# Kernel tuning notes

Hardware: AMD Instinct MI355X
Metric: run time of the kernel (lower is better)

The kernel has to match this reference:

```python
import jax, jax.numpy as jnp
import numpy as np

B, C, U, LEN, K = 32, 16, 16, 128, 4  # batch, channels, units, image side, cheb order
POWERS = K + 1


def _path_chebyshev(n, k):
    """Chebyshev polynomials T_0..T_k of the rescaled normalized Laplacian of an
    undirected path graph with n nodes. Returns [k+1, n, n] float32."""
    A = np.zeros((n, n), dtype=np.float64)
    A[np.arange(n - 1), np.arange(1, n)] = 1.0
    A = A + A.T
    d = A.sum(axis=1)
    dinv = 1.0 / np.sqrt(d)
    L = np.eye(n) - dinv[:, None] * A * dinv[None, :]   # normalized Laplacian
    Lt = L - np.eye(n)                                   # rescaled: 2L/lambda_max - I, lambda_max=2
    T = [np.eye(n), Lt]
    for _ in range(2, k + 1):
        T.append(2.0 * Lt @ T[-1] - T[-2])
    return np.stack(T[: k + 1]).astype(np.float32)


def setup_inputs() -> dict:
    key = jax.random.key(0)
    kx, kc = jax.random.split(key)
    x = jax.random.normal(kx, (B, C, LEN, LEN), dtype=jnp.float32)
    coefs = 0.001 * jax.random.normal(kc, (POWERS, POWERS, C, U), dtype=jnp.float32)
    cheb = jnp.asarray(_path_chebyshev(LEN, K))  # same graph for both axes
    return {"x": x, "coefs": coefs, "cheb1": cheb, "cheb2": cheb}


def reference(x, coefs, cheb1, cheb2):
    # out[b,u,p,q] = sum_{k1,k2,c,h,w} coefs[k1,k2,c,u] * cheb1[k1,h,p] * x[b,c,h,w] * cheb2[k2,w,q]
    t1 = jnp.einsum('bchw,khp->bkcpw', x, cheb1)        # apply cheb1 along H
    s = jnp.einsum('bkcpw,klcu->blupw', t1, coefs)      # contract k1 and channels
    out = jnp.einsum('blupw,lwq->bupq', s, cheb2)       # apply cheb2 along W, contract k2
    return out
```

## Files before the change

### kernel.cpp

```cpp
#include <hip/hip_runtime.h>
#include <hip/hip_bf16.h>

#define LEN 128
#define NB 32
#define NC 16
#define NU 16
#define NK 5
#define KC 80
#define KCP 96

typedef unsigned int uint32;
typedef unsigned short ushort16;
typedef __attribute__((ext_vector_type(8))) short bf16x8;
typedef __attribute__((ext_vector_type(4))) float f32x4;

#define MFMA(a, b, c) __builtin_amdgcn_mfma_f32_16x16x32_bf16(a, b, c, 0, 0, 0)

#define SIG(r) (((r) & 15) ^ (((r) >> 3) & 15))

static __device__ inline ushort16 f2bf(float f) {
    union { float f; uint32 u; } v; v.f = f;
    uint32 u = v.u;
    uint32 r = (u + 0x7fffu + ((u >> 16) & 1u)) >> 16;
    return (ushort16)r;
}
static __device__ inline uint32 pkbf(float a, float b) {
    return (uint32)f2bf(a) | ((uint32)f2bf(b) << 16);
}
static __device__ inline bf16x8 frag16(const void* p) {
    return *(const bf16x8*)p;
}

__global__ __launch_bounds__(256) void kprep(const float* __restrict__ x,
                                             const float* __restrict__ coefs,
                                             const float* __restrict__ cheb1,
                                             const float* __restrict__ cheb2,
                                             ushort16* __restrict__ xF,
                                             ushort16* __restrict__ cheb1F,
                                             ushort16* __restrict__ cheb2F,
                                             ushort16* __restrict__ coefF) {
    __shared__ __align__(16) uint32 Xs[128 * 64];
    const int blk = blockIdx.x, tid = threadIdx.x;
    if (blk < 512) {
        const int bc = blk;
        const float* xp = x + (size_t)bc * (LEN * LEN);
        {
            int w = tid & 127, hg = tid >> 7;
            #pragma unroll
            for (int uu = 0; uu < 8; ++uu) {
                int u = hg * 8 + uu;
                uint4 d;
                uint32* dp = (uint32*)&d;
                #pragma unroll
                for (int t = 0; t < 4; ++t) {
                    int h2 = u * 4 + t;
                    dp[t] = pkbf(xp[(2 * h2) * LEN + w], xp[(2 * h2 + 1) * LEN + w]);
                }
                *(uint4*)(Xs + w * 64 + ((u ^ SIG(w)) << 2)) = d;
            }
        }
        __syncthreads();
        ushort16* dst = xF + (size_t)bc * 16384;
        #pragma unroll
        for (int i = 0; i < 8; ++i) {
            int n = tid + i * 256;
            int lane = n & 63, fk = n >> 6;
            int wrow = (fk >> 2) * 16 + (lane & 15);
            int u = (fk & 3) * 4 + (lane >> 4);
            uint4 v = *(const uint4*)(Xs + wrow * 64 + ((u ^ SIG(wrow)) << 2));
            *(uint4*)(dst + (size_t)n * 8) = v;
        }
    } else {
        int i = (blk - 512) * 256 + tid;
        if (i < 81920) {
            int j = i & 7, lane = (i >> 3) & 63, ks = (i >> 9) & 3, nt = i >> 11;
            int kp = nt * 16 + (lane & 15);
            int k = kp >> 7, p = kp & 127;
            int h = ks * 32 + ((lane >> 4) << 3) + j;
            cheb1F[i] = f2bf(cheb1[(k * LEN + h) * LEN + p]);
        } else if (i < 163840) {
            int i2 = i - 81920;
            int j = i2 & 7, lane = (i2 >> 3) & 63, t = i2 >> 9;
            int ks = t % 20, nt = t / 20;
            int q = nt * 16 + (lane & 15);
            int lw = ks * 32 + ((lane >> 4) << 3) + j;
            int l = lw >> 7, w = lw & 127;
            cheb2F[i2] = f2bf(cheb2[(l * LEN + w) * LEN + q]);
        } else {
            int i3 = i - 163840;
            int j = i3 & 7, lane = (i3 >> 3) & 63, t = i3 >> 9;
            int ks = t % 3, nt = t / 3;
            int lu = nt * 16 + (lane & 15);
            int l = lu >> 4, u = lu & 15;
            int kc = ks * 32 + ((lane >> 4) << 3) + j;
            int k = kc >> 4, c = kc & 15;
            coefF[i3] = (kc < KC) ? f2bf(coefs[((k * NK + l) * NC + c) * NU + u]) : (ushort16)0;
        }
    }
}

__global__ __launch_bounds__(256, 4) void k1_mfma(const ushort16* __restrict__ xF,
                                                  const ushort16* __restrict__ cheb1F,
                                                  const float* __restrict__ x,
                                                  ushort16* __restrict__ t1, int b0) {
    __shared__ __align__(16) uint32 Ls[64 * 64];
    __shared__ __align__(16) uint32 Bs[64 * 64];
    const int c = blockIdx.x, bl = blockIdx.y, z = blockIdx.z;
    const int b = b0 + bl;
    const int tid = threadIdx.x;
    const int lane = tid & 63, wave = tid >> 6;
    const int m16 = lane & 15, g = lane >> 4;
    const int wm = wave >> 1, wn = wave & 1;

    #pragma unroll
    for (int i = 0; i < 4; ++i) {
        int u = tid + i * 256;
        int ln = u & 63, ks = (u >> 6) & 3, nt = u >> 8;
        uint4 v = *(const uint4*)(cheb1F + ((size_t)(((8 + z * 4 + nt) * 4 + ks) * 64 + ln)) * 8);
        int row = nt * 16 + (ln & 15), hu = ks * 4 + (ln >> 4);
        *(uint4*)(Ls + row * 64 + ((hu ^ SIG(row)) << 2)) = v;
    }

    if (z == 0) {
        const float* xp = x + (size_t)(b * NC + c) * (LEN * LEN);
        int p = tid >> 1, half = tid & 1;
        const float4* src = (const float4*)(xp + p * LEN + half * 64);
        ushort16* dst = t1 + ((size_t)(bl * LEN + p) * KC + c) * LEN + half * 64;
        #pragma unroll
        for (int i = 0; i < 16; ++i) {
            float4 v = src[i];
            uint2 d;
            d.x = pkbf(v.x, v.y);
            d.y = pkbf(v.z, v.w);
            *(uint2*)(dst + i * 4) = d;
        }
    }
    __syncthreads();

    const ushort16* xFb = xF + ((size_t)(b * NC + c)) * 16384;

    f32x4 acc[4][2];
    #pragma unroll
    for (int mi = 0; mi < 4; ++mi)
        #pragma unroll
        for (int ni = 0; ni < 2; ++ni) acc[mi][ni] = (f32x4)0.f;

    #pragma unroll
    for (int ks = 0; ks < 4; ++ks) {
        bf16x8 Af[4], Bf[2];
        #pragma unroll
        for (int mi = 0; mi < 4; ++mi) {
            int mt = wm * 4 + mi;
            Af[mi] = frag16(xFb + ((size_t)(mt * 4 + ks) * 64 + lane) * 8);
        }
        #pragma unroll
        for (int ni = 0; ni < 2; ++ni) {
            int row = (wn * 2 + ni) * 16 + m16;
            int hu = ks * 4 + g;
            Bf[ni] = frag16(Ls + row * 64 + ((hu ^ SIG(row)) << 2));
        }
        #pragma unroll
        for (int mi = 0; mi < 4; ++mi)
            #pragma unroll
            for (int ni = 0; ni < 2; ++ni)
                acc[mi][ni] = MFMA(Af[mi], Bf[ni], acc[mi][ni]);
    }

    #pragma unroll
    for (int ni = 0; ni < 2; ++ni)
        #pragma unroll
        for (int mi = 0; mi < 4; ++mi) {
            int rr = (wn * 2 + ni) * 16 + m16;
            int wu = (wm * 4 + mi) * 16 + g * 4;
            uint2 d;
            d.x = pkbf(acc[mi][ni][0], acc[mi][ni][1]);
            d.y = pkbf(acc[mi][ni][2], acc[mi][ni][3]);
            int u = wu >> 3;
            *(uint2*)(Bs + rr * 64 + ((u ^ SIG(rr)) << 2) + ((wu >> 1) & 3)) = d;
        }
    __syncthreads();

    #pragma unroll
    for (int i = 0; i < 4; ++i) {
        int n = tid + i * 256;
        int rr = n >> 4, wsg = n & 15;
        uint4 v = *(const uint4*)(Bs + rr * 64 + ((wsg ^ SIG(rr)) << 2));
        int kp = 128 + z * 64 + rr;
        int k = kp >> 7, p = kp & 127;
        *(uint4*)(t1 + ((size_t)((bl * LEN + p) * KC + k * NC + c)) * LEN + wsg * 8) = v;
    }
}

__global__ __launch_bounds__(256, 5) void k2_mfma(const ushort16* __restrict__ t1,
                                                  const ushort16* __restrict__ coefF,
                                                  const ushort16* __restrict__ cheb2F,
                                                  float* __restrict__ out, int b0) {
    __shared__ __align__(16) uint32 sm[128 * 64];
    const int p = blockIdx.x, bl = blockIdx.y, b = b0 + bl;
    const int tid = threadIdx.x;
    const int lane = tid & 63, wave = tid >> 6;
    const int n16 = lane & 15, g = lane >> 4;

    const uint32* t1u = (const uint32*)(t1 + (size_t)(bl * LEN + p) * (KC * LEN));
    uint4 Av[3], Bv[3];
    #pragma unroll
    for (int i = 0; i < 3; ++i) {
        int it = tid + i * 256;
        if (it < 640) {
            int a2 = it >> 4, wq = it & 15;
            const uint32* src = t1u + a2 * 128 + wq * 4;
            Av[i] = *(const uint4*)(src);
            Bv[i] = *(const uint4*)(src + 64);
        }
    }
    #pragma unroll
    for (int i = 0; i < 4; ++i) {
        int idx = tid + i * 256;
        int row = idx >> 3, d = idx & 7;
        int u = 10 + (d >> 2);
        sm[row * 64 + ((u ^ SIG(row)) << 2) + (d & 3)] = 0;
    }
    #pragma unroll
    for (int i = 0; i < 3; ++i) {
        int it = tid + i * 256;
        if (it < 640) {
            int a2 = it >> 4, wq = it & 15;
            const uint32* av = (const uint32*)&Av[i];
            const uint32* bv = (const uint32*)&Bv[i];
            int u = a2 >> 2, lo = a2 & 3;
            #pragma unroll
            for (int j = 0; j < 4; ++j) {
                int r0 = wq * 8 + 2 * j, r1 = r0 + 1;
                sm[r0 * 64 + ((u ^ SIG(r0)) << 2) + lo] = (av[j] & 0xffffu) | (bv[j] << 16);
                sm[r1 * 64 + ((u ^ SIG(r1)) << 2) + lo] = (av[j] >> 16) | (bv[j] & 0xffff0000u);
            }
        }
    }
    __syncthreads();

    f32x4 acc[2][5];
    #pragma unroll
    for (int mi = 0; mi < 2; ++mi)
        #pragma unroll
        for (int ni = 0; ni < 5; ++ni) acc[mi][ni] = (f32x4)0.f;

    #pragma unroll
    for (int ks = 0; ks < 3; ++ks) {
        bf16x8 Af[2], Bf[5];
        #pragma unroll
        for (int mi = 0; mi < 2; ++mi) {
            int row = wave * 32 + mi * 16 + n16;
            Af[mi] = frag16(sm + row * 64 + (((ks * 4 + g) ^ SIG(row)) << 2));
        }
        #pragma unroll
        for (int ni = 0; ni < 5; ++ni)
            Bf[ni] = frag16(coefF + ((size_t)(ni * 3 + ks) * 64 + lane) * 8);
        #pragma unroll
        for (int mi = 0; mi < 2; ++mi)
            #pragma unroll
            for (int ni = 0; ni < 5; ++ni)
                acc[mi][ni] = MFMA(Af[mi], Bf[ni], acc[mi][ni]);
    }
    __syncthreads();

    {
        ushort16* A3 = (ushort16*)sm;
        #pragma unroll
        for (int mi = 0; mi < 2; ++mi)
            #pragma unroll
            for (int ni = 0; ni < 5; ++ni) {
                int wcol = wave * 32 + mi * 16 + g * 4;
                uint2 d;
                d.x = pkbf(acc[mi][ni][0], acc[mi][ni][1]);
                d.y = pkbf(acc[mi][ni][2], acc[mi][ni][3]);
                *(uint2*)(A3 + n16 * 648 + ni * 128 + wcol) = d;
            }
    }
    __syncthreads();

    const ushort16* A3r = (const ushort16*)sm;
    f32x4 c3[2];
    c3[0] = (f32x4)0.f; c3[1] = (f32x4)0.f;
    #pragma unroll 4
    for (int ks = 4; ks < 20; ++ks) {
        bf16x8 Aa = frag16(A3r + n16 * 648 + ks * 32 + g * 8);
        #pragma unroll
        for (int nt = 0; nt < 2; ++nt) {
            bf16x8 Bb = frag16(cheb2F + ((size_t)((wave * 2 + nt) * 20 + ks) * 64 + lane) * 8);
            c3[nt] = MFMA(Aa, Bb, c3[nt]);
        }
    }

    #pragma unroll
    for (int nt = 0; nt < 2; ++nt)
        #pragma unroll
        for (int r = 0; r < 4; ++r) {
            int u = g * 4 + r;
            int q = wave * 32 + nt * 16 + n16;
            uint32 bf = ((uint32)A3r[u * 648 + q]) << 16;
            float l0 = __uint_as_float(bf);
            out[(((size_t)(b * NU + u)) * LEN + p) * LEN + q] = c3[nt][r] + l0;
        }
}

extern "C" void kernel_launch(void* const* d_in, const int* in_sizes, int n_in,
                              void* d_out, int out_size, void* d_ws, size_t ws_size,
                              hipStream_t stream) {
    const float* x     = (const float*)d_in[0];
    const float* coefs = (const float*)d_in[1];
    const float* cheb1 = (const float*)d_in[2];
    const float* cheb2 = (const float*)d_in[3];
    float* out = (float*)d_out;

    const size_t xF_bytes  = (size_t)NB * NC * 16384 * sizeof(ushort16);
    const size_t aux_bytes = 163840 + 163840 + 15360;
    size_t off = (ws_size - aux_bytes - xF_bytes) & ~(size_t)255;
    ushort16* cheb1F = (ushort16*)((char*)d_ws + off);
    ushort16* cheb2F = cheb1F + 81920;
    ushort16* coefF  = cheb2F + 81920;
    ushort16* xF     = coefF + 7680;
    ushort16* t1 = (ushort16*)d_ws;

    const size_t per_b = (size_t)LEN * KC * LEN * sizeof(ushort16);
    int chunk = (int)(off / per_b);
    if (chunk < 1) chunk = 1;
    if (chunk > NB) chunk = NB;

    hipLaunchKernelGGL(kprep, dim3(1182), dim3(256), 0, stream,
                       x, coefs, cheb1, cheb2, xF, cheb1F, cheb2F, coefF);
    for (int b0 = 0; b0 < NB; b0 += chunk) {
        int cb = (NB - b0 < chunk) ? (NB - b0) : chunk;
        hipLaunchKernelGGL(k1_mfma, dim3(NC, cb, 8), dim3(256), 0, stream,
                           xF, cheb1F, x, t1, b0);
        hipLaunchKernelGGL(k2_mfma, dim3(LEN, cb), dim3(256), 0, stream,
                           t1, coefF, cheb2F, out, b0);
    }
}
```

Baseline: 152.6 us.

## Process two p rows per k2 block with cheb2 fragments held in registers

Each k2 block now handles two consecutive p rows instead of one, halving the grid. The cheb2 B fragments are loaded into 32 registers once per block and reused across both rows. The t1 loads for the second row are issued during the first row's compute to overlap memory latency. Launch bounds drop to 2 blocks per SM to fit the much larger register footprint, which reduces occupancy and latency hiding.

```diff
diff --git a/kernel.cpp b/kernel.cpp
--- a/kernel.cpp
+++ b/kernel.cpp
@@ -191,116 +191,142 @@
     }
 }
 
-__global__ __launch_bounds__(256, 5) void k2_mfma(const ushort16* __restrict__ t1,
+__global__ __launch_bounds__(256, 2) void k2_mfma(const ushort16* __restrict__ t1,
                                                   const ushort16* __restrict__ coefF,
                                                   const ushort16* __restrict__ cheb2F,
                                                   float* __restrict__ out, int b0) {
     __shared__ __align__(16) uint32 sm[128 * 64];
-    const int p = blockIdx.x, bl = blockIdx.y, b = b0 + bl;
+    const int pblk = blockIdx.x, bl = blockIdx.y, b = b0 + bl;
     const int tid = threadIdx.x;
     const int lane = tid & 63, wave = tid >> 6;
     const int n16 = lane & 15, g = lane >> 4;
 
-    const uint32* t1u = (const uint32*)(t1 + (size_t)(bl * LEN + p) * (KC * LEN));
+    bf16x8 B3[32];
+    #pragma unroll
+    for (int nt = 0; nt < 2; ++nt)
+        #pragma unroll
+        for (int ks = 4; ks < 20; ++ks)
+            B3[nt * 16 + ks - 4] =
+                frag16(cheb2F + ((size_t)((wave * 2 + nt) * 20 + ks) * 64 + lane) * 8);
+
+    const uint32* t1base = (const uint32*)(t1 + (size_t)(bl * LEN + 2 * pblk) * (KC * LEN));
+
     uint4 Av[3], Bv[3];
     #pragma unroll
     for (int i = 0; i < 3; ++i) {
         int it = tid + i * 256;
         if (it < 640) {
             int a2 = it >> 4, wq = it & 15;
-            const uint32* src = t1u + a2 * 128 + wq * 4;
+            const uint32* src = t1base + a2 * 128 + wq * 4;
             Av[i] = *(const uint4*)(src);
             Bv[i] = *(const uint4*)(src + 64);
         }
     }
-    #pragma unroll
-    for (int i = 0; i < 4; ++i) {
-        int idx = tid + i * 256;
-        int row = idx >> 3, d = idx & 7;
-        int u = 10 + (d >> 2);
-        sm[row * 64 + ((u ^ SIG(row)) << 2) + (d & 3)] = 0;
-    }
-    #pragma unroll
-    for (int i = 0; i < 3; ++i) {
-        int it = tid + i * 256;
-        if (it < 640) {
-            int a2 = it >> 4, wq = it & 15;
-            const uint32* av = (const uint32*)&Av[i];
-            const uint32* bv = (const uint32*)&Bv[i];
-            int u = a2 >> 2, lo = a2 & 3;
-            #pragma unroll
-            for (int j = 0; j < 4; ++j) {
-                int r0 = wq * 8 + 2 * j, r1 = r0 + 1;
-                sm[r0 * 64 + ((u ^ SIG(r0)) << 2) + lo] = (av[j] & 0xffffu) | (bv[j] << 16);
-                sm[r1 * 64 + ((u ^ SIG(r1)) << 2) + lo] = (av[j] >> 16) | (bv[j] & 0xffff0000u);
-            }
-        }
-    }
-    __syncthreads();
-
-    f32x4 acc[2][5];
-    #pragma unroll
-    for (int mi = 0; mi < 2; ++mi)
-        #pragma unroll
-        for (int ni = 0; ni < 5; ++ni) acc[mi][ni] = (f32x4)0.f;
-
-    #pragma unroll
-    for (int ks = 0; ks < 3; ++ks) {
-        bf16x8 Af[2], Bf[5];
-        #pragma unroll
-        for (int mi = 0; mi < 2; ++mi) {
-            int row = wave * 32 + mi * 16 + n16;
-            Af[mi] = frag16(sm + row * 64 + (((ks * 4 + g) ^ SIG(row)) << 2));
-        }
-        #pragma unroll
-        for (int ni = 0; ni < 5; ++ni)
-            Bf[ni] = frag16(coefF + ((size_t)(ni * 3 + ks) * 64 + lane) * 8);
+
+    #pragma unroll
+    for (int pi = 0; pi < 2; ++pi) {
+        const int p = 2 * pblk + pi;
+        if (pi) __syncthreads();
+
+        #pragma unroll
+        for (int i = 0; i < 4; ++i) {
+            int idx = tid + i * 256;
+            int row = idx >> 3, d = idx & 7;
+            int u = 10 + (d >> 2);
+            sm[row * 64 + ((u ^ SIG(row)) << 2) + (d & 3)] = 0;
+        }
+        #pragma unroll
+        for (int i = 0; i < 3; ++i) {
+            int it = tid + i * 256;
+            if (it < 640) {
+                int a2 = it >> 4, wq = it & 15;
+                const uint32* av = (const uint32*)&Av[i];
+                const uint32* bv = (const uint32*)&Bv[i];
+                int u = a2 >> 2, lo = a2 & 3;
+                #pragma unroll
+                for (int j = 0; j < 4; ++j) {
+                    int r0 = wq * 8 + 2 * j, r1 = r0 + 1;
+                    sm[r0 * 64 + ((u ^ SIG(r0)) << 2) + lo] = (av[j] & 0xffffu) | (bv[j] << 16);
+                    sm[r1 * 64 + ((u ^ SIG(r1)) << 2) + lo] = (av[j] >> 16) | (bv[j] & 0xffff0000u);
+                }
+            }
+        }
+        __syncthreads();
+
+        if (pi == 0) {
+            #pragma unroll
+            for (int i = 0; i < 3; ++i) {
+                int it = tid + i * 256;
+                if (it < 640) {
+                    int a2 = it >> 4, wq = it & 15;
+                    const uint32* src = t1base + 5120 + a2 * 128 + wq * 4;
+                    Av[i] = *(const uint4*)(src);
+                    Bv[i] = *(const uint4*)(src + 64);
+                }
+            }
+        }
+
+        f32x4 acc[2][5];
         #pragma unroll
         for (int mi = 0; mi < 2; ++mi)
             #pragma unroll
+            for (int ni = 0; ni < 5; ++ni) acc[mi][ni] = (f32x4)0.f;
+
+        #pragma unroll
+        for (int ks = 0; ks < 3; ++ks) {
+            bf16x8 Af[2], Bf[5];
+            #pragma unroll
+            for (int mi = 0; mi < 2; ++mi) {
+                int row = wave * 32 + mi * 16 + n16;
+                Af[mi] = frag16(sm + row * 64 + (((ks * 4 + g) ^ SIG(row)) << 2));
+            }
+            #pragma unroll
             for (int ni = 0; ni < 5; ++ni)
-                acc[mi][ni] = MFMA(Af[mi], Bf[ni], acc[mi][ni]);
-    }
-    __syncthreads();
-
-    {
-        ushort16* A3 = (ushort16*)sm;
-        #pragma unroll
-        for (int mi = 0; mi < 2; ++mi)
-            #pragma unroll
-            for (int ni = 0; ni < 5; ++ni) {
-                int wcol = wave * 32 + mi * 16 + g * 4;
-                uint2 d;
-                d.x = pkbf(acc[mi][ni][0], acc[mi][ni][1]);
-                d.y = pkbf(acc[mi][ni][2], acc[mi][ni][3]);
-                *(uint2*)(A3 + n16 * 648 + ni * 128 + wcol) = d;
-            }
-    }
-    __syncthreads();
-
-    const ushort16* A3r = (const ushort16*)sm;
-    f32x4 c3[2];
-    c3[0] = (f32x4)0.f; c3[1] = (f32x4)0.f;
-    #pragma unroll 4
-    for (int ks = 4; ks < 20; ++ks) {
-        bf16x8 Aa = frag16(A3r + n16 * 648 + ks * 32 + g * 8);
-        #pragma unroll
-        for (int nt = 0; nt < 2; ++nt) {
-            bf16x8 Bb = frag16(cheb2F + ((size_t)((wave * 2 + nt) * 20 + ks) * 64 + lane) * 8);
-            c3[nt] = MFMA(Aa, Bb, c3[nt]);
-        }
-    }
-
-    #pragma unroll
-    for (int nt = 0; nt < 2; ++nt)
-        #pragma unroll
-        for (int r = 0; r < 4; ++r) {
-            int u = g * 4 + r;
-            int q = wave * 32 + nt * 16 + n16;
-            uint32 bf = ((uint32)A3r[u * 648 + q]) << 16;
-            float l0 = __uint_as_float(bf);
-            out[(((size_t)(b * NU + u)) * LEN + p) * LEN + q] = c3[nt][r] + l0;
-        }
+                Bf[ni] = frag16(coefF + ((size_t)(ni * 3 + ks) * 64 + lane) * 8);
+            #pragma unroll
+            for (int mi = 0; mi < 2; ++mi)
+                #pragma unroll
+                for (int ni = 0; ni < 5; ++ni)
+                    acc[mi][ni] = MFMA(Af[mi], Bf[ni], acc[mi][ni]);
+        }
+        __syncthreads();
+
+        {
+            ushort16* A3 = (ushort16*)sm;
+            #pragma unroll
+            for (int mi = 0; mi < 2; ++mi)
+                #pragma unroll
+                for (int ni = 0; ni < 5; ++ni) {
+                    int wcol = wave * 32 + mi * 16 + g * 4;
+                    uint2 d;
+                    d.x = pkbf(acc[mi][ni][0], acc[mi][ni][1]);
+                    d.y = pkbf(acc[mi][ni][2], acc[mi][ni][3]);
+                    *(uint2*)(A3 + n16 * 648 + ni * 128 + wcol) = d;
+                }
+        }
+        __syncthreads();
+
+        const ushort16* A3r = (const ushort16*)sm;
+        f32x4 c3[2];
+        c3[0] = (f32x4)0.f; c3[1] = (f32x4)0.f;
+        #pragma unroll
+        for (int ks = 4; ks < 20; ++ks) {
+            bf16x8 Aa = frag16(A3r + n16 * 648 + ks * 32 + g * 8);
+            c3[0] = MFMA(Aa, B3[ks - 4], c3[0]);
+            c3[1] = MFMA(Aa, B3[16 + ks - 4], c3[1]);
+        }
+
+        #pragma unroll
+        for (int nt = 0; nt < 2; ++nt)
+            #pragma unroll
+            for (int r = 0; r < 4; ++r) {
+                int u = g * 4 + r;
+                int q = wave * 32 + nt * 16 + n16;
+                uint32 bf = ((uint32)A3r[u * 648 + q]) << 16;
+                float l0 = __uint_as_float(bf);
+                out[(((size_t)(b * NU + u)) * LEN + p) * LEN + q] = c3[nt][r] + l0;
+            }
+    }
 }
 
 extern "C" void kernel_launch(void* const* d_in, const int* in_sizes, int n_in,
@@ -332,7 +358,7 @@
         int cb = (NB - b0 < chunk) ? (NB - b0) : chunk;
         hipLaunchKernelGGL(k1_mfma, dim3(NC, cb, 8), dim3(256), 0, stream,
                            xF, cheb1F, x, t1, b0);
-        hipLaunchKernelGGL(k2_mfma, dim3(LEN, cb), dim3(256), 0, stream,
+        hipLaunchKernelGGL(k2_mfma, dim3(64, cb), dim3(256), 0, stream,
                            t1, coefF, cheb2F, out, b0);
     }
 }
```

Result: no change. 155.1 us (+1.6%).
